# Optimization experiments

Hardware: AMD Instinct MI355X
Metric: run time of the kernel (lower is better)

The kernel has to match this reference:

```python
import jax, jax.numpy as jnp
import numpy as np

D_MODEL = 2048
N_HEADS = 32
N_KV = 8
HEAD_DIM = D_MODEL // N_HEADS  # 64
D_FF = 8192
ROPE_BASE = 10000.0
EPS = 1e-5
B, S = 2, 2048


def setup_inputs() -> dict:
    key = jax.random.key(0)
    ks = jax.random.split(key, 8)
    s = 0.02
    qkv_out = (N_HEADS + 2 * N_KV) * HEAD_DIM
    return {
        "x": jax.random.normal(ks[0], (B, S, D_MODEL), jnp.float32),
        "w_norm1": jnp.ones((D_MODEL,), jnp.float32),
        "w_qkv": jax.random.normal(ks[1], (D_MODEL, qkv_out), jnp.float32) * s,
        "w_out": jax.random.normal(ks[2], (D_MODEL, D_MODEL), jnp.float32) * s,
        "w_norm2": jnp.ones((D_MODEL,), jnp.float32),
        "w_gate": jax.random.normal(ks[3], (D_MODEL, D_FF), jnp.float32) * s,
        "w_up": jax.random.normal(ks[4], (D_MODEL, D_FF), jnp.float32) * s,
        "w_down": jax.random.normal(ks[5], (D_FF, D_MODEL), jnp.float32) * s,
    }


def _rmsnorm(x, w):
    var = jnp.mean(x * x, axis=-1, keepdims=True)
    return x * jax.lax.rsqrt(var + EPS) * w


def _rope(x, cos, sin):
    # x: [b, s, h, d]; cos/sin: [s, d/2]; non-interleaved (NeoX half split)
    half = x.shape[-1] // 2
    x1, x2 = x[..., :half], x[..., half:]
    c = cos[None, :, None, :]
    sn = sin[None, :, None, :]
    return jnp.concatenate([x1 * c - x2 * sn, x1 * sn + x2 * c], axis=-1)


def _forward(x, w_norm1, w_qkv, w_out, w_norm2, w_gate, w_up, w_down):
    b, s, d = x.shape
    # --- attention block ---
    h = _rmsnorm(x, w_norm1)
    qkv = h @ w_qkv  # [b, s, (H + 2*KV) * hd]
    q = qkv[..., : N_HEADS * HEAD_DIM].reshape(b, s, N_HEADS, HEAD_DIM)
    kv = qkv[..., N_HEADS * HEAD_DIM:].reshape(b, s, 2, N_KV, HEAD_DIM)
    k, v = kv[:, :, 0], kv[:, :, 1]

    inv_freq = 1.0 / (ROPE_BASE ** (jnp.arange(0, HEAD_DIM, 2, dtype=jnp.float32) / HEAD_DIM))
    t = jnp.arange(s, dtype=jnp.float32)
    freqs = t[:, None] * inv_freq[None, :]  # [s, hd/2]
    cos, sin = jnp.cos(freqs), jnp.sin(freqs)
    q = _rope(q, cos, sin)
    k = _rope(k, cos, sin)

    # GQA: repeat_interleave kv heads to match q heads
    g = N_HEADS // N_KV
    k = jnp.repeat(k, g, axis=2)  # [b, s, H, hd]
    v = jnp.repeat(v, g, axis=2)

    scale = 1.0 / np.sqrt(HEAD_DIM)
    scores = jnp.einsum("bqhd,bkhd->bhqk", q, k) * scale
    causal = jnp.tril(jnp.ones((s, s), bool))
    scores = jnp.where(causal[None, None], scores, jnp.finfo(scores.dtype).min)
    attn = jax.nn.softmax(scores, axis=-1)
    ctx = jnp.einsum("bhqk,bkhd->bqhd", attn, v).reshape(b, s, N_HEADS * HEAD_DIM)
    x = x + ctx @ w_out

    # --- MLP block (SwiGLU) ---
    h2 = _rmsnorm(x, w_norm2)
    mlp = (jax.nn.silu(h2 @ w_gate) * (h2 @ w_up)) @ w_down
    return x + mlp


def reference(x, w_norm1, w_qkv, w_out, w_norm2, w_gate, w_up, w_down):
    return _forward(x, w_norm1, w_qkv, w_out, w_norm2, w_gate, w_up, w_down)
```

## Files before the change

kernel.cpp:

```cpp
#include <hip/hip_runtime.h>
#include <stdint.h>

#define D_MODEL 2048
#define S_LEN   2048
#define NTOK    4096
#define QKV_N   3072
#define DFF     8192

typedef float  f32x4   __attribute__((ext_vector_type(4)));
typedef float  f32x16  __attribute__((ext_vector_type(16)));
typedef __bf16 bf16x8  __attribute__((ext_vector_type(8)));
typedef unsigned short u16;
typedef unsigned short u16x8 __attribute__((ext_vector_type(8)));

__device__ __forceinline__ float b2f(u16 u){ union{float f; uint32_t i;} v; v.i = ((uint32_t)u) << 16; return v.f; }
__device__ __forceinline__ u16 f2b(float f){
  union{float f; uint32_t i;} v; v.f = f;
  uint32_t r = v.i + 0x7FFFu + ((v.i >> 16) & 1u);
  return (u16)(r >> 16);
}

__device__ __forceinline__ void gload_lds16(const void* gsrc, void* ldst){
  __builtin_amdgcn_global_load_lds(
      (const __attribute__((address_space(1))) void*)gsrc,
      (__attribute__((address_space(3))) void*)ldst,
      16, 0, 0);
}

__device__ __forceinline__ void conv_tiles(const float* W, const float* W2, u16* WT,
    int Nfull, int Kt, int Nt, int k0g, int n0g, int rmul, void* ldsbuf)
{
  if (W == nullptr) return;
  float* tf = (float*)ldsbuf;
  const int tt  = threadIdx.x;
  const int nTn = Nt >> 6;
  const int nT  = (Kt >> 6) * nTn;
  const int bid = (blockIdx.z * gridDim.y + blockIdx.y) * gridDim.x + blockIdx.x;
  const int gsz = gridDim.x * gridDim.y * gridDim.z;
  const int c4 = (tt & 15) << 2;
  const int r  = tt >> 4;
  for (int tile = bid; tile < nT; tile += gsz) {
    const int k0 = (tile / nTn) << 6, n0 = (tile % nTn) << 6;
    for (int m = 0; m < 2; ++m) {
      const float* Ws = m ? W2 : W;
      if (m && W2 == nullptr) break;
      __syncthreads();
      if (tt < 256) {
#pragma unroll
        for (int i = 0; i < 4; ++i) {
          int row = r + i * 16;
          float4 v = *reinterpret_cast<const float4*>(&Ws[(size_t)(k0g + k0 + row) * Nfull + n0g + n0 + c4]);
          tf[row * 65 + c4 + 0] = v.x; tf[row * 65 + c4 + 1] = v.y;
          tf[row * 65 + c4 + 2] = v.z; tf[row * 65 + c4 + 3] = v.w;
        }
      }
      __syncthreads();
      if (tt < 256) {
#pragma unroll
        for (int i = 0; i < 4; ++i) {
          int n = r + i * 16;
          ushort4 ov;
          ov.x = f2b(tf[(c4 + 0) * 65 + n]); ov.y = f2b(tf[(c4 + 1) * 65 + n]);
          ov.z = f2b(tf[(c4 + 2) * 65 + n]); ov.w = f2b(tf[(c4 + 3) * 65 + n]);
          *reinterpret_cast<ushort4*>(&WT[(size_t)((n0 + n) * rmul + m) * Kt + k0 + c4]) = ov;
        }
      }
    }
  }
}

__global__ void sincos_kernel(float* __restrict__ ct, float* __restrict__ st)
{
  int idx = blockIdx.x * 256 + threadIdx.x;
  if (idx >= S_LEN * 32) return;
  int p = idx >> 5, i = idx & 31;
  double freq = pow(10000.0, -((double)(2*i)) / 64.0);
  double ang  = (double)p * freq;
  ct[idx] = (float)cos(ang);
  st[idx] = (float)sin(ang);
}

template<bool BF16IN>
__global__ __launch_bounds__(256) void rmsnorm_kernel(const void* __restrict__ xin, const float* __restrict__ w, u16* __restrict__ out,
                                                      const float* cvW, const float* cvW2, u16* cvWT, int cvNfull, int cvKt, int cvNt, int cvK0g, int cvN0g, int cvRm)
{
  __shared__ float tfbuf[64 * 65];
  const int row = blockIdx.x;
  const int t = threadIdx.x;
  float v[8];
  if (BF16IN) {
    const u16* xr = ((const u16*)xin) + (size_t)row * D_MODEL;
    u16x8 a = *reinterpret_cast<const u16x8*>(&xr[t*8]);
#pragma unroll
    for (int j = 0; j < 8; ++j) v[j] = b2f(a[j]);
  } else {
    const float* xr = ((const float*)xin) + (size_t)row * D_MODEL;
    float4 a = *reinterpret_cast<const float4*>(&xr[t*8]);
    float4 c = *reinterpret_cast<const float4*>(&xr[t*8+4]);
    v[0]=a.x; v[1]=a.y; v[2]=a.z; v[3]=a.w; v[4]=c.x; v[5]=c.y; v[6]=c.z; v[7]=c.w;
  }
  float ss = 0.f;
#pragma unroll
  for (int j = 0; j < 8; ++j) ss += v[j]*v[j];
#pragma unroll
  for (int d = 1; d < 64; d <<= 1) ss += __shfl_xor(ss, d);
  __shared__ float red[4];
  if ((t & 63) == 0) red[t >> 6] = ss;
  __syncthreads();
  ss = red[0] + red[1] + red[2] + red[3];
  const float sc = rsqrtf(ss * (1.0f / (float)D_MODEL) + 1e-5f);
  float4 w0 = *reinterpret_cast<const float4*>(&w[t*8]);
  float4 w1 = *reinterpret_cast<const float4*>(&w[t*8+4]);
  u16x8 o;
  o[0]=f2b(v[0]*sc*w0.x); o[1]=f2b(v[1]*sc*w0.y); o[2]=f2b(v[2]*sc*w0.z); o[3]=f2b(v[3]*sc*w0.w);
  o[4]=f2b(v[4]*sc*w1.x); o[5]=f2b(v[5]*sc*w1.y); o[6]=f2b(v[6]*sc*w1.z); o[7]=f2b(v[7]*sc*w1.w);
  *reinterpret_cast<u16x8*>(&out[(size_t)row * D_MODEL + t*8]) = o;
  conv_tiles(cvW, cvW2, cvWT, cvNfull, cvKt, cvNt, cvK0g, cvN0g, cvRm, tfbuf);
}

template<int EPI>
__device__ __forceinline__ void epi_store(size_t idx, float v, float* Cf, u16* Cb,
                                          const float* resf, const u16* resb, const u16* other)
{
  if (EPI == 2)      Cb[idx] = f2b(v / (1.0f + __expf(-v)));
  else if (EPI == 3) Cb[idx] = f2b(v * b2f(other[idx]));
  else if (EPI == 4) Cb[idx] = f2b(v);
  else if (EPI == 5) Cf[idx] += v;
  else if (EPI == 6) Cb[idx] = f2b(v + resf[idx]);
  else if (EPI == 7) Cf[idx] = v + b2f(resb[idx]);
  else if (EPI == 9) {
    float pv = __shfl_xor(v, 1);
    float gate = (threadIdx.x & 1) ? pv : v;
    float up   = (threadIdx.x & 1) ? v  : pv;
    if (!(threadIdx.x & 1)) Cb[idx] = f2b(gate / (1.0f + __expf(-gate)) * up);
  }
}

template<int EPI>
__global__ __launch_bounds__(512, 2) void gemm8p_kernel(
    const u16* __restrict__ A, const u16* __restrict__ BT, const u16* __restrict__ BT2,
    int K, int lda, int ldb, int ldc, int n_off,
    float* Cf, u16* Cb,
    const float* __restrict__ resf, const u16* __restrict__ resb, const u16* other,
    const float* cvW, const float* cvW2, u16* cvWT, int cvNfull, int cvKt, int cvNt, int cvK0g, int cvN0g, int cvRm)
{
  __shared__ u16 lds[65536];
  const int tid = threadIdx.x;
  const int w = tid >> 6, lane = tid & 63;
  const int g = lane >> 4, lr = lane & 15;
  const int wm = w >> 2, wn = w & 3;
  int fid = blockIdx.y * gridDim.x + blockIdx.x;
  const int nwg = gridDim.x * gridDim.y;
  fid = (fid & 7) * (nwg >> 3) + (fid >> 3);
  const int bn = fid / gridDim.y, bm = fid % gridDim.y;
  const int NT = K >> 6;
  const int NI = NT >> 1;

  const int srow = tid >> 3;
  const int sg   = (tid & 7) ^ (srow & 7);
  const u16* Asrc = A + (size_t)(bm * 256) * lda;
  const u16* Bsrc;
  if (EPI == 9) Bsrc = (bn < 16) ? BT + (size_t)(bn * 256) * ldb
                                 : BT2 + (size_t)(bn * 256 - 4096) * ldb;
  else          Bsrc = BT + (size_t)(bn * 256) * ldb;

  const int agc0 = ((0 + g) ^ (lr & 7)) * 8;
  const int agc1 = ((4 + g) ^ (lr & 7)) * 8;

  f32x4 acc[8][4];
#pragma unroll
  for (int i = 0; i < 8; ++i)
#pragma unroll
    for (int j = 0; j < 4; ++j) acc[i][j] = (f32x4){0.f, 0.f, 0.f, 0.f};
  bf16x8 af[4][2], bf0[2][2], bf1[2][2];

#define STAGE_H(isB, h, b, T) do {                                           \
    int tc = ((T) < NT) ? (T) : (NT - 1);                                    \
    const u16* sb = (isB) ? Bsrc : Asrc;                                     \
    const int  sld = (isB) ? ldb : lda;                                      \
    const u16* s0 = sb + (size_t)((h)*128 + srow) * sld + tc*64 + sg*8;      \
    u16* dst = &lds[(b)*32768 + (isB)*16384 + (h)*8192 + tid*8];             \
    gload_lds16(s0, dst);                                                    \
    gload_lds16(s0 + (size_t)64 * sld, dst + 4096);                          \
  } while (0)

#define LOADA(mih, b) { _Pragma("unroll") for (int q = 0; q < 4; ++q) {      \
    const u16* rp = &lds[(b)*32768 + (wm*128 + (mih)*64 + q*16 + lr) * 64];  \
    af[q][0] = *(const bf16x8*)(rp + agc0);                                  \
    af[q][1] = *(const bf16x8*)(rp + agc1); } }

#define LOADB(dst, nih, b) { _Pragma("unroll") for (int nq = 0; nq < 2; ++nq) { \
    const u16* rp = &lds[(b)*32768 + 16384 + (wn*64 + (nih)*32 + nq*16 + lr) * 64]; \
    dst[nq][0] = *(const bf16x8*)(rp + agc0);                                \
    dst[nq][1] = *(const bf16x8*)(rp + agc1); } }

#define MM(mih, nih, BF) {                                                   \
    __builtin_amdgcn_s_setprio(1);                                           \
    _Pragma("unroll") for (int kk = 0; kk < 2; ++kk)                         \
      _Pragma("unroll") for (int q = 0; q < 4; ++q)                          \
        _Pragma("unroll") for (int nq = 0; nq < 2; ++nq)                     \
          acc[(mih)*4+q][(nih)*2+nq] = __builtin_amdgcn_mfma_f32_16x16x32_bf16( \
              af[q][kk], BF[nq][kk], acc[(mih)*4+q][(nih)*2+nq], 0, 0, 0);   \
    __builtin_amdgcn_s_setprio(0); }

#define PHEND     __builtin_amdgcn_s_barrier();
#define PHEND_VM  asm volatile("s_waitcnt vmcnt(4)" ::: "memory");           \
                  __builtin_amdgcn_s_barrier();

  STAGE_H(0, 0, 0, 0); STAGE_H(0, 1, 0, 0);
  STAGE_H(1, 0, 0, 0); STAGE_H(1, 1, 0, 0);
  STAGE_H(1, 0, 1, 1); STAGE_H(1, 1, 1, 1);
  asm volatile("s_waitcnt vmcnt(4)" ::: "memory");
  __builtin_amdgcn_s_barrier();

  for (int i = 0; i < NI; ++i) {
    const int t0 = 2 * i;
    LOADA(0, 0); LOADB(bf0, 0, 0);
    STAGE_H(0, 0, 1, t0 + 1);
    MM(0, 0, bf0); PHEND;
    LOADB(bf1, 1, 0);
    STAGE_H(0, 1, 1, t0 + 1);
    MM(0, 1, bf1); PHEND;
    LOADA(1, 0);
    STAGE_H(1, 0, 0, t0 + 2);
    MM(1, 1, bf1); PHEND;
    STAGE_H(1, 1, 0, t0 + 2);
    MM(1, 0, bf0); PHEND_VM;
    LOADA(0, 1); LOADB(bf0, 0, 1);
    STAGE_H(0, 0, 0, t0 + 2);
    MM(0, 0, bf0); PHEND;
    LOADB(bf1, 1, 1);
    STAGE_H(0, 1, 0, t0 + 2);
    MM(0, 1, bf1); PHEND;
    LOADA(1, 1);
    STAGE_H(1, 0, 1, t0 + 3);
    MM(1, 1, bf1); PHEND;
    STAGE_H(1, 1, 1, t0 + 3);
    MM(1, 0, bf0); PHEND_VM;
  }
#undef STAGE_H
#undef LOADA
#undef LOADB
#undef MM

#pragma unroll
  for (int mi = 0; mi < 8; ++mi) {
    const int rowOff = (mi >> 2) * 64 + (mi & 3) * 16;
#pragma unroll
    for (int ni = 0; ni < 4; ++ni) {
      const int colOff = (ni >> 1) * 32 + (ni & 1) * 16;
#pragma unroll
      for (int j = 0; j < 4; ++j) {
        int row = bm*256 + wm*128 + rowOff + g*4 + j;
        int col = n_off + bn*256 + wn*64 + colOff + lr;
        size_t idx = (EPI == 9) ? ((size_t)row * ldc + (col >> 1))
                                : ((size_t)row * ldc + col);
        epi_store<EPI>(idx, acc[mi][ni][j], Cf, Cb, resf, resb, other);
      }
    }
  }
  conv_tiles(cvW, cvW2, cvWT, cvNfull, cvKt, cvNt, cvK0g, cvN0g, cvRm, lds);
}

template<int EPI>
__global__ __launch_bounds__(512) void gemm128_kernel(
    const u16* __restrict__ A, const u16* __restrict__ BT,
    int K, int lda, int ldb, int ldc, int n_off,
    float* Cf, u16* Cb,
    const float* __restrict__ resf, const u16* __restrict__ resb, const u16* other,
    const float* c1W, const float* c1W2, u16* c1WT, int c1Nfull, int c1Kt, int c1Nt, int c1K0g, int c1N0g, int c1Rm,
    const float* c2W, const float* c2W2, u16* c2WT, int c2Nfull, int c2Kt, int c2Nt, int c2K0g, int c2N0g, int c2Rm)
{
  __shared__ u16 lds[49152];
  const int tid = threadIdx.x;
  const int w = tid >> 6, lane = tid & 63;
  const int g = lane >> 4, lr = lane & 15;
  const int wm = w >> 2, wn = w & 3;
  int fid = blockIdx.y * gridDim.x + blockIdx.x;
  const int nwg = gridDim.x * gridDim.y;
  fid = (fid & 7) * (nwg >> 3) + (fid >> 3);
  const int bn = fid / gridDim.y, bm = fid % gridDim.y;
  const int NT = K >> 6;
  const int NI = NT >> 1;

  const int srow = tid >> 3;
  const int sg   = (tid & 7) ^ (srow & 7);
  const u16* Asrc = A  + (size_t)(bm * 128) * lda;
  const u16* Bsrc = BT + (size_t)(bn * 256) * ldb;

  const int agc0 = ((0 + g) ^ (lr & 7)) * 8;
  const int agc1 = ((4 + g) ^ (lr & 7)) * 8;

  f32x4 acc[4][4];
#pragma unroll
  for (int i = 0; i < 4; ++i)
#pragma unroll
    for (int j = 0; j < 4; ++j) acc[i][j] = (f32x4){0.f, 0.f, 0.f, 0.f};
  bf16x8 af[2][2], bf0[2][2], bf1[2][2];

#define STAGE_A(b, T) do {                                                   \
    int tc = ((T) < NT) ? (T) : (NT - 1);                                    \
    const u16* s0 = Asrc + (size_t)srow * lda + tc*64 + sg*8;                \
    u16* dst = &lds[(b)*24576 + tid*8];                                      \
    gload_lds16(s0, dst);                                                    \
    gload_lds16(s0 + (size_t)64 * lda, dst + 4096);                          \
  } while (0)

#define STAGE_BH(h, b, T) do {                                               \
    int tc = ((T) < NT) ? (T) : (NT - 1);                                    \
    const u16* s0 = Bsrc + (size_t)((h)*128 + srow) * ldb + tc*64 + sg*8;    \
    u16* dst = &lds[(b)*24576 + 8192 + (h)*8192 + tid*8];                    \
    gload_lds16(s0, dst);                                                    \
    gload_lds16(s0 + (size_t)64 * ldb, dst + 4096);                         \
  } while (0)

#define LOADA(mih, b) { _Pragma("unroll") for (int q = 0; q < 2; ++q) {      \
    const u16* rp = &lds[(b)*24576 + (wm*64 + (mih)*32 + q*16 + lr) * 64];   \
    af[q][0] = *(const bf16x8*)(rp + agc0);                                  \
    af[q][1] = *(const bf16x8*)(rp + agc1); } }

#define LOADB(dst, nih, b) { _Pragma("unroll") for (int nq = 0; nq < 2; ++nq) { \
    const u16* rp = &lds[(b)*24576 + 8192 + (wn*64 + (nih)*32 + nq*16 + lr) * 64]; \
    dst[nq][0] = *(const bf16x8*)(rp + agc0);                                \
    dst[nq][1] = *(const bf16x8*)(rp + agc1); } }

#define MM(mih, nih, BF) {                                                   \
    __builtin_amdgcn_s_setprio(1);                                           \
    _Pragma("unroll") for (int kk = 0; kk < 2; ++kk)                         \
      _Pragma("unroll") for (int q = 0; q < 2; ++q)                          \
        _Pragma("unroll") for (int nq = 0; nq < 2; ++nq)                     \
          acc[(mih)*2+q][(nih)*2+nq] = __builtin_amdgcn_mfma_f32_16x16x32_bf16( \
              af[q][kk], BF[nq][kk], acc[(mih)*2+q][(nih)*2+nq], 0, 0, 0);   \
    __builtin_amdgcn_s_setprio(0); }

#define PHEND     __builtin_amdgcn_s_barrier();

  STAGE_A(0, 0); STAGE_BH(0, 0, 0); STAGE_BH(1, 0, 0);
  STAGE_BH(0, 1, 1); STAGE_BH(1, 1, 1);
  asm volatile("s_waitcnt vmcnt(4)" ::: "memory");
  __builtin_amdgcn_s_barrier();

  for (int i = 0; i < NI; ++i) {
    const int t0 = 2 * i;
    LOADA(0, 0); LOADB(bf0, 0, 0);
    STAGE_A(1, t0 + 1);
    MM(0, 0, bf0); PHEND;
    LOADB(bf1, 1, 0);
    STAGE_BH(0, 0, t0 + 2);
    MM(0, 1, bf1); PHEND;
    LOADA(1, 0);
    STAGE_BH(1, 0, t0 + 2);
    MM(1, 1, bf1); PHEND;
    STAGE_A(0, t0 + 2);
    MM(1, 0, bf0);
    asm volatile("s_waitcnt vmcnt(6)" ::: "memory");
    __builtin_amdgcn_s_barrier();
    LOADA(0, 1); LOADB(bf0, 0, 1);
    MM(0, 0, bf0); PHEND;
    LOADB(bf1, 1, 1);
    STAGE_BH(0, 1, t0 + 3);
    MM(0, 1, bf1); PHEND;
    LOADA(1, 1);
    STAGE_BH(1, 1, t0 + 3);
    MM(1, 1, bf1); PHEND;
    MM(1, 0, bf0);
    asm volatile("s_waitcnt vmcnt(4)" ::: "memory");
    __builtin_amdgcn_s_barrier();
  }
#undef STAGE_A
#undef STAGE_BH
#undef LOADA
#undef LOADB
#undef MM
#undef PHEND

#pragma unroll
  for (int mi = 0; mi < 4; ++mi) {
    const int rowOff = (mi >> 1) * 32 + (mi & 1) * 16;
#pragma unroll
    for (int ni = 0; ni < 4; ++ni) {
      const int colOff = (ni >> 1) * 32 + (ni & 1) * 16;
#pragma unroll
      for (int j = 0; j < 4; ++j) {
        int row = bm*128 + wm*64 + rowOff + g*4 + j;
        int col = n_off + bn*256 + wn*64 + colOff + lr;
        epi_store<EPI>((size_t)row * ldc + col, acc[mi][ni][j], Cf, Cb, resf, resb, other);
      }
    }
  }
  conv_tiles(c1W, c1W2, c1WT, c1Nfull, c1Kt, c1Nt, c1K0g, c1N0g, c1Rm, lds);
  conv_tiles(c2W, c2W2, c2WT, c2Nfull, c2Kt, c2Nt, c2K0g, c2N0g, c2Rm, lds);
}

__global__ __launch_bounds__(256) void rope_kernel(
    const u16* __restrict__ qkv, const float* __restrict__ ct, const float* __restrict__ st,
    u16* __restrict__ Kt, u16* __restrict__ VT)
{
  const int tok = blockIdx.x;
  const int b = tok >> 11, s = tok & (S_LEN - 1);
  const int w = threadIdx.x >> 6, lane = threadIdx.x & 63;
  const size_t base = (size_t)tok * QKV_N;
  for (int slot = w; slot < 16; slot += 4) {
    int col = (slot < 8) ? 2048 + slot * 64 : 2560 + (slot - 8) * 64;
    float v = b2f(qkv[base + col + lane]);
    if (slot < 8) {
      int i = lane & 31;
      float c = ct[s * 32 + i], sn = st[s * 32 + i];
      float p = b2f(qkv[base + col + (lane ^ 32)]);
      v = (lane < 32) ? (v * c - p * sn) : (v * c + p * sn);
    }
    u16 ob = f2b(v);
    if (slot < 8) Kt[((size_t)(b * 8 + slot)     * S_LEN + s) * 64 + lane] = ob;
    else          VT[((size_t)(b * 8 + slot - 8) * 64 + lane) * S_LEN + s] = ob;
  }
}

#define ASCALE 0.1803368801111204f
#define MFIX   16.0f
__global__ __launch_bounds__(256, 2) void attn_kernel(
    const u16* __restrict__ qkv, const u16* __restrict__ Kt,
    const u16* __restrict__ VT, u16* __restrict__ ctx,
    const float* __restrict__ ct, const float* __restrict__ st,
    const float* cvW, const float* cvW2, u16* cvWT, int cvNfull, int cvKt, int cvNt, int cvK0g, int cvN0g, int cvRm)
{
  __shared__ float tfbuf[64 * 65];
  const int fid = blockIdx.y * gridDim.x + blockIdx.x;
  const int idx = fid >> 3;
  const int bh  = (fid & 7) * 8 + (idx & 7);
  const int y   = idx >> 3;
  const int wid = threadIdx.x >> 6;
  const int lane = threadIdx.x & 63;
  const int b = bh >> 5, h = bh & 31;
  const int kvh = (b << 3) + (h >> 2);
  const int jj = y * 4 + wid;
  const int cq = lane & 31;
  const int hi = lane >> 5;

  const u16* Kp = Kt + (size_t)kvh * S_LEN * 64 + cq * 64 + hi * 8;
  const u16* Vbase = VT + (size_t)kvh * 64 * S_LEN + hi * 8;
  const u16* Vp[4];
#pragma unroll
  for (int v = 0; v < 4; ++v)
    Vp[v] = Vbase + (size_t)((v & 1) * 32 + cq) * S_LEN + (v >> 1) * 16;

  __shared__ float xch[4][32];

#define ATT_LOADK(KF, T) { _Pragma("unroll") for (int q_ = 0; q_ < 4; ++q_) \
    KF[q_] = *(const bf16x8*)(Kp + (T) * 2048 + q_ * 16); }
#define ATT_LOADV(VF, T) { _Pragma("unroll") for (int v_ = 0; v_ < 4; ++v_) \
    VF[v_] = *(const bf16x8*)(Vp[v_] + (T) * 32); }

#define ATT_QK(S, KF) do {                                                   \
    S = (f32x16){};                                                          \
    S = __builtin_amdgcn_mfma_f32_32x32x16_bf16(KF[0], qf[0], S, 0, 0, 0);   \
    S = __builtin_amdgcn_mfma_f32_32x32x16_bf16(KF[1], qf[1], S, 0, 0, 0);   \
    S = __builtin_amdgcn_mfma_f32_32x32x16_bf16(KF[2], qf[2], S, 0, 0, 0);   \
    S = __builtin_amdgcn_mfma_f32_32x32x16_bf16(KF[3], qf[3], S, 0, 0, 0);   \
  } while (0)

#define ATT_PACK(P, PA0, PA1) do {                                           \
    uint32_t wds[8], pw[8];                                                  \
    _Pragma("unroll") for (int j = 0; j < 8; ++j) {                          \
      uint32_t wv;                                                           \
      asm("v_cvt_pk_bf16_f32 %0, %1, %2" : "=v"(wv) : "v"((P)[2*j]), "v"((P)[2*j+1])); \
      wds[j] = wv;                                                           \
    }                                                                        \
    _Pragma("unroll") for (int j = 0; j < 8; ++j) pw[j] = __shfl_xor(wds[j], 32); \
    PA0.u[0] = hi ? pw[2]  : wds[0];                                         \
    PA0.u[1] = hi ? pw[3]  : wds[1];                                         \
    PA0.u[2] = hi ? wds[2] : pw[0];                                          \
    PA0.u[3] = hi ? wds[3] : pw[1];                                          \
    PA1.u[0] = hi ? pw[6]  : wds[4];                                         \
    PA1.u[1] = hi ? pw[7]  : wds[5];                                         \
    PA1.u[2] = hi ? wds[6] : pw[4];                                          \
    PA1.u[3] = hi ? wds[7] : pw[5];                                          \
  } while (0)

#define ATT_FIN1(S, VF) do {                                                 \
    float p[16];                                                             \
    _Pragma("unroll") for (int r = 0; r < 16; ++r) p[r] = S[r];              \
    _Pragma("unroll") for (int r = 0; r < 16; ++r) {                         \
      int kk = (r & 3) + 8 * (r >> 2) + 4 * hi;                              \
      if (kk > cq) p[r] = -1e30f;                                            \
    }                                                                        \
    float ts_ = 0.f;                                                         \
    _Pragma("unroll") for (int r = 0; r < 16; ++r) { p[r] = exp2f(p[r] - MFIX); ts_ += p[r]; } \
    l += ts_;                                                                \
    union { uint32_t u[4]; bf16x8 v; } pa0, pa1;                             \
    ATT_PACK(p, pa0, pa1);                                                   \
    o0 = __builtin_amdgcn_mfma_f32_32x32x16_bf16(pa0.v, VF[0], o0, 0, 0, 0); \
    o0 = __builtin_amdgcn_mfma_f32_32x32x16_bf16(pa1.v, VF[2], o0, 0, 0, 0); \
    o1 = __builtin_amdgcn_mfma_f32_32x32x16_bf16(pa0.v, VF[1], o1, 0, 0, 0); \
    o1 = __builtin_amdgcn_mfma_f32_32x32x16_bf16(pa1.v, VF[3], o1, 0, 0, 0); \
  } while (0)

#define ATT_FIN2(SA, SB, VFA, VFB, MASKB) do {                               \
    float p[32];                                                             \
    _Pragma("unroll") for (int r = 0; r < 16; ++r) { p[r] = SA[r]; p[16+r] = SB[r]; } \
    if (MASKB) {                                                             \
      _Pragma("unroll") for (int r = 0; r < 16; ++r) {                       \
        int kk = (r & 3) + 8 * (r >> 2) + 4 * hi;                            \
        if (kk > cq) p[16+r] = -1e30f;                                       \
      }                                                                      \
    }                                                                        \
    _Pragma("unroll") for (int r = 0; r < 32; ++r) p[r] = exp2f(p[r] - MFIX); \
    {                                                                        \
      float s1_ = 0.f, s2_ = 0.f;                                            \
      _Pragma("unroll") for (int r = 0; r < 16; ++r) { s1_ += p[r]; s2_ += p[16+r]; } \
      l += s1_ + s2_;                                                        \
    }                                                                        \
    union { uint32_t u[4]; bf16x8 v; } pa0, pa1, pb0, pb1;                   \
    ATT_PACK(p, pa0, pa1);                                                   \
    ATT_PACK((p + 16), pb0, pb1);                                            \
    o0 = __builtin_amdgcn_mfma_f32_32x32x16_bf16(pa0.v, VFA[0], o0, 0, 0, 0); \
    o0 = __builtin_amdgcn_mfma_f32_32x32x16_bf16(pa1.v, VFA[2], o0, 0, 0, 0); \
    o1 = __builtin_amdgcn_mfma_f32_32x32x16_bf16(pa0.v, VFA[1], o1, 0, 0, 0); \
    o1 = __builtin_amdgcn_mfma_f32_32x32x16_bf16(pa1.v, VFA[3], o1, 0, 0, 0); \
    o0 = __builtin_amdgcn_mfma_f32_32x32x16_bf16(pb0.v, VFB[0], o0, 0, 0, 0); \
    o0 = __builtin_amdgcn_mfma_f32_32x32x16_bf16(pb1.v, VFB[2], o0, 0, 0, 0); \
    o1 = __builtin_amdgcn_mfma_f32_32x32x16_bf16(pb0.v, VFB[1], o1, 0, 0, 0); \
    o1 = __builtin_amdgcn_mfma_f32_32x32x16_bf16(pb1.v, VFB[3], o1, 0, 0, 0); \
  } while (0)

#pragma unroll 1
  for (int task = 0; task < 2; ++task) {
    const int qt = task ? (63 - jj) : jj;
    const int q0 = qt << 5;
    const int nt = qt + 1;

    bf16x8 qf[4];
    {
      const u16* Qr = qkv + (size_t)(b * S_LEN + q0 + cq) * QKV_N + h * 64 + hi * 8;
      u16 qr[4][8];
#pragma unroll
      for (int t = 0; t < 4; ++t)
        *reinterpret_cast<u16x8*>(qr[t]) = *reinterpret_cast<const u16x8*>(Qr + t * 16);
      const float* cb = ct + (size_t)(q0 + cq) * 32 + hi * 8;
      const float* sb = st + (size_t)(q0 + cq) * 32 + hi * 8;
      union { u16 u[8]; bf16x8 v; } qo[4];
#pragma unroll
      for (int t = 0; t < 2; ++t) {
        float4 c0 = *reinterpret_cast<const float4*>(cb + 16 * t);
        float4 c1 = *reinterpret_cast<const float4*>(cb + 16 * t + 4);
        float4 s0 = *reinterpret_cast<const float4*>(sb + 16 * t);
        float4 s1 = *reinterpret_cast<const float4*>(sb + 16 * t + 4);
        float cc[8] = {c0.x,c0.y,c0.z,c0.w, c1.x,c1.y,c1.z,c1.w};
        float ssn[8] = {s0.x,s0.y,s0.z,s0.w, s1.x,s1.y,s1.z,s1.w};
#pragma unroll
        for (int i = 0; i < 8; ++i) {
          float lo = b2f(qr[t][i]), hif = b2f(qr[t + 2][i]);
          qo[t].u[i]     = f2b((lo * cc[i] - hif * ssn[i]) * ASCALE);
          qo[t + 2].u[i] = f2b((hif * cc[i] + lo * ssn[i]) * ASCALE);
        }
      }
#pragma unroll
      for (int t = 0; t < 4; ++t) qf[t] = qo[t].v;
    }

    f32x16 o0 = {}, o1 = {};
    float l = 0.f;

    const int npair = nt >> 1;
    bf16x8 kfA[4], kfB[4], vfA[4], vfB[4];

#pragma unroll 1
    for (int i = 0; i < npair; ++i) {
      const int Ta = 2 * i, Tb = 2 * i + 1;
      ATT_LOADK(kfA, Ta); ATT_LOADK(kfB, Tb);
      ATT_LOADV(vfA, Ta); ATT_LOADV(vfB, Tb);
      f32x16 sA, sB;
      ATT_QK(sA, kfA); ATT_QK(sB, kfB);
      ATT_FIN2(sA, sB, vfA, vfB, (Tb == nt - 1));
    }
    if (nt & 1) {
      const int T = nt - 1;
      ATT_LOADK(kfA, T); ATT_LOADV(vfA, T);
      f32x16 sA;
      ATT_QK(sA, kfA);
      ATT_FIN1(sA, vfA);
    }

    l += __shfl_xor(l, 32);
    float linv = 1.0f / l;
    if (hi == 0) xch[wid][cq] = linv;
    asm volatile("s_waitcnt lgkmcnt(0)" ::: "memory");
    __builtin_amdgcn_sched_barrier(0);
    float4 n0 = *reinterpret_cast<const float4*>(&xch[wid][4 * hi + 0]);
    float4 n1 = *reinterpret_cast<const float4*>(&xch[wid][4 * hi + 8]);
    float4 n2 = *reinterpret_cast<const float4*>(&xch[wid][4 * hi + 16]);
    float4 n3 = *reinterpret_cast<const float4*>(&xch[wid][4 * hi + 24]);
    float na[16] = {n0.x,n0.y,n0.z,n0.w, n1.x,n1.y,n1.z,n1.w,
                    n2.x,n2.y,n2.z,n2.w, n3.x,n3.y,n3.z,n3.w};
#pragma unroll
    for (int r = 0; r < 16; ++r) {
      int row = (r & 3) + 8 * (r >> 2) + 4 * hi;
      size_t base = (size_t)(b * S_LEN + q0 + row) * D_MODEL + h * 64;
      ctx[base + cq]      = f2b(o0[r] * na[r]);
      ctx[base + 32 + cq] = f2b(o1[r] * na[r]);
    }
  }
#undef ATT_LOADK
#undef ATT_LOADV
#undef ATT_QK
#undef ATT_PACK
#undef ATT_FIN1
#undef ATT_FIN2

  conv_tiles(cvW, cvW2, cvWT, cvNfull, cvKt, cvNt, cvK0g, cvN0g, cvRm, tfbuf);
}

#define NOCV nullptr, nullptr, nullptr, 0, 0, 0, 0, 0, 1
extern "C" void kernel_launch(void* const* d_in, const int* in_sizes, int n_in,
                              void* d_out, int out_size, void* d_ws, size_t ws_size,
                              hipStream_t stream)
{
  const float* x     = (const float*)d_in[0];
  const float* wn1   = (const float*)d_in[1];
  const float* wqkv  = (const float*)d_in[2];
  const float* wout  = (const float*)d_in[3];
  const float* wn2   = (const float*)d_in[4];
  const float* wgate = (const float*)d_in[5];
  const float* wup   = (const float*)d_in[6];
  const float* wdown = (const float*)d_in[7];
  float* out = (float*)d_out;
  char* ws = (char*)d_ws;

  float* cosT = (float*)(ws + 0);
  float* sinT = (float*)(ws + 262144);
  u16*   U1   = (u16*)  (ws + 524288);
  u16*   U2   = (u16*)  (ws + 17301504);
  u16*   x1b  = (u16*)  (ws + 34078720);
  char*  S    = ws + 50855936;
  u16*   hB   = (u16*)(S + 0);
  u16*   qkvB = (u16*)(S + 16777216);
  u16*   kB   = (u16*)(S + 41943040);
  u16*   vtB  = (u16*)(S + 46137344);
  u16*   ctxB = (u16*)(S + 0);
  u16*   h2B  = (u16*)(S + 0);
  u16*   slab = (u16*)(S + 16777216);
  u16*   U7   = (u16*)(S + 50331648);

  sincos_kernel<<<dim3(256), 256, 0, stream>>>(cosT, sinT);
  rmsnorm_kernel<false><<<dim3(NTOK), 256, 0, stream>>>(x, wn1, hB,
      wqkv, nullptr, U1, 3072, 2048, 3072, 0, 0, 1);

  gemm128_kernel<4><<<dim3(12, 32), 512, 0, stream>>>(hB, U1, 2048, 2048, 2048, 3072, 0,
      nullptr, qkvB, nullptr, nullptr, nullptr,
      wout, nullptr, U7, 2048, 2048, 2048, 0, 0, 1, NOCV);
  rope_kernel<<<dim3(NTOK), 256, 0, stream>>>(qkvB, cosT, sinT, kB, vtB);
  attn_kernel<<<dim3(64, 8), 256, 0, stream>>>(qkvB, kB, vtB, ctxB, cosT, sinT,
      wgate, wup, U1, 8192, 2048, 2048, 0, 0, 2);

  gemm128_kernel<6><<<dim3(8, 32), 512, 0, stream>>>(ctxB, U7, 2048, 2048, 2048, 2048, 0,
      nullptr, x1b, x, nullptr, nullptr,
      wgate, wup, U2, 8192, 2048, 2048, 0, 2048, 2, NOCV);

  rmsnorm_kernel<true><<<dim3(NTOK), 256, 0, stream>>>(x1b, wn2, h2B,
      wdown, nullptr, U7, 2048, 4096, 2048, 0, 0, 1);

  gemm8p_kernel<9><<<dim3(32, 16), 512, 0, stream>>>(h2B, U1, U2, 2048, 2048, 2048, 4096, 0,
      nullptr, slab, nullptr, nullptr, nullptr, NOCV);
  gemm128_kernel<7><<<dim3(8, 32), 512, 0, stream>>>(slab, U7, 4096, 4096, 4096, 2048, 0,
      out, nullptr, nullptr, x1b, nullptr,
      wgate, wup, U1, 8192, 2048, 2048, 0, 4096, 2,
      wgate, wup, U2, 8192, 2048, 2048, 0, 6144, 2);
  gemm8p_kernel<9><<<dim3(32, 16), 512, 0, stream>>>(h2B, U1, U2, 2048, 2048, 2048, 4096, 0,
      nullptr, slab, nullptr, nullptr, nullptr,
      wdown, nullptr, U7, 2048, 4096, 2048, 4096, 0, 1);
  gemm128_kernel<5><<<dim3(8, 32), 512, 0, stream>>>(slab, U7, 4096, 4096, 4096, 2048, 0,
      out, nullptr, nullptr, nullptr, nullptr, NOCV, NOCV);
}
```

Measured before the change: 766.8 us.

## Fuse paired causal query tiles to share K/V loads in attention

Each wave previously handled its two balanced query tiles (jj and 63-jj) one after the other, loading K and V separately for each. Now both tiles' Q fragments are loaded up front and a single loop over key tiles runs, so every K/V fragment is loaded once and used by both query tiles. This removes redundant global K/V traffic but drops the two-tile unroll that gave more instruction-level parallelism. It also doubles the live accumulator registers, which may lower occupancy.

```diff
diff --git a/kernel.cpp b/kernel.cpp
--- a/kernel.cpp
+++ b/kernel.cpp
@@ -436,6 +436,9 @@
   const int cq = lane & 31;
   const int hi = lane >> 5;
 
+  const int q0a = jj << 5,        nta = jj + 1;
+  const int q0b = (63 - jj) << 5, ntb = 64 - jj;
+
   const u16* Kp = Kt + (size_t)kvh * S_LEN * 64 + cq * 64 + hi * 8;
   const u16* Vbase = VT + (size_t)kvh * 64 * S_LEN + hi * 8;
   const u16* Vp[4];
@@ -450,12 +453,12 @@
 #define ATT_LOADV(VF, T) { _Pragma("unroll") for (int v_ = 0; v_ < 4; ++v_) \
     VF[v_] = *(const bf16x8*)(Vp[v_] + (T) * 32); }
 
-#define ATT_QK(S, KF) do {                                                   \
+#define ATT_QK(S, KF, QF) do {                                               \
     S = (f32x16){};                                                          \
-    S = __builtin_amdgcn_mfma_f32_32x32x16_bf16(KF[0], qf[0], S, 0, 0, 0);   \
-    S = __builtin_amdgcn_mfma_f32_32x32x16_bf16(KF[1], qf[1], S, 0, 0, 0);   \
-    S = __builtin_amdgcn_mfma_f32_32x32x16_bf16(KF[2], qf[2], S, 0, 0, 0);   \
-    S = __builtin_amdgcn_mfma_f32_32x32x16_bf16(KF[3], qf[3], S, 0, 0, 0);   \
+    S = __builtin_amdgcn_mfma_f32_32x32x16_bf16(KF[0], QF[0], S, 0, 0, 0);   \
+    S = __builtin_amdgcn_mfma_f32_32x32x16_bf16(KF[1], QF[1], S, 0, 0, 0);   \
+    S = __builtin_amdgcn_mfma_f32_32x32x16_bf16(KF[2], QF[2], S, 0, 0, 0);   \
+    S = __builtin_amdgcn_mfma_f32_32x32x16_bf16(KF[3], QF[3], S, 0, 0, 0);   \
   } while (0)
 
 #define ATT_PACK(P, PA0, PA1) do {                                           \
@@ -476,135 +479,100 @@
     PA1.u[3] = hi ? wds[7] : pw[5];                                          \
   } while (0)
 
-#define ATT_FIN1(S, VF) do {                                                 \
+#define ATT_FIN(S, VF, O0, O1, L, MASK) do {                                 \
     float p[16];                                                             \
     _Pragma("unroll") for (int r = 0; r < 16; ++r) p[r] = S[r];              \
-    _Pragma("unroll") for (int r = 0; r < 16; ++r) {                         \
-      int kk = (r & 3) + 8 * (r >> 2) + 4 * hi;                              \
-      if (kk > cq) p[r] = -1e30f;                                            \
+    if (MASK) {                                                              \
+      _Pragma("unroll") for (int r = 0; r < 16; ++r) {                       \
+        int kk = (r & 3) + 8 * (r >> 2) + 4 * hi;                            \
+        if (kk > cq) p[r] = -1e30f;                                          \
+      }                                                                      \
     }                                                                        \
     float ts_ = 0.f;                                                         \
     _Pragma("unroll") for (int r = 0; r < 16; ++r) { p[r] = exp2f(p[r] - MFIX); ts_ += p[r]; } \
-    l += ts_;                                                                \
+    L += ts_;                                                                \
     union { uint32_t u[4]; bf16x8 v; } pa0, pa1;                             \
     ATT_PACK(p, pa0, pa1);                                                   \
-    o0 = __builtin_amdgcn_mfma_f32_32x32x16_bf16(pa0.v, VF[0], o0, 0, 0, 0); \
-    o0 = __builtin_amdgcn_mfma_f32_32x32x16_bf16(pa1.v, VF[2], o0, 0, 0, 0); \
-    o1 = __builtin_amdgcn_mfma_f32_32x32x16_bf16(pa0.v, VF[1], o1, 0, 0, 0); \
-    o1 = __builtin_amdgcn_mfma_f32_32x32x16_bf16(pa1.v, VF[3], o1, 0, 0, 0); \
-  } while (0)
-
-#define ATT_FIN2(SA, SB, VFA, VFB, MASKB) do {                               \
-    float p[32];                                                             \
-    _Pragma("unroll") for (int r = 0; r < 16; ++r) { p[r] = SA[r]; p[16+r] = SB[r]; } \
-    if (MASKB) {                                                             \
-      _Pragma("unroll") for (int r = 0; r < 16; ++r) {                       \
-        int kk = (r & 3) + 8 * (r >> 2) + 4 * hi;                            \
-        if (kk > cq) p[16+r] = -1e30f;                                       \
+    O0 = __builtin_amdgcn_mfma_f32_32x32x16_bf16(pa0.v, VF[0], O0, 0, 0, 0); \
+    O0 = __builtin_amdgcn_mfma_f32_32x32x16_bf16(pa1.v, VF[2], O0, 0, 0, 0); \
+    O1 = __builtin_amdgcn_mfma_f32_32x32x16_bf16(pa0.v, VF[1], O1, 0, 0, 0); \
+    O1 = __builtin_amdgcn_mfma_f32_32x32x16_bf16(pa1.v, VF[3], O1, 0, 0, 0); \
+  } while (0)
+
+#define ATT_LOADQ(QF, Q0) do {                                               \
+    const u16* Qr = qkv + (size_t)(b * S_LEN + (Q0) + cq) * QKV_N + h * 64 + hi * 8; \
+    u16 qr[4][8];                                                            \
+    _Pragma("unroll") for (int t = 0; t < 4; ++t)                            \
+      *reinterpret_cast<u16x8*>(qr[t]) = *reinterpret_cast<const u16x8*>(Qr + t * 16); \
+    const float* cb = ct + (size_t)((Q0) + cq) * 32 + hi * 8;                \
+    const float* sb = st + (size_t)((Q0) + cq) * 32 + hi * 8;                \
+    union { u16 u[8]; bf16x8 v; } qo[4];                                     \
+    _Pragma("unroll") for (int t = 0; t < 2; ++t) {                          \
+      float4 c0 = *reinterpret_cast<const float4*>(cb + 16 * t);             \
+      float4 c1 = *reinterpret_cast<const float4*>(cb + 16 * t + 4);         \
+      float4 s0 = *reinterpret_cast<const float4*>(sb + 16 * t);             \
+      float4 s1 = *reinterpret_cast<const float4*>(sb + 16 * t + 4);         \
+      float cc[8] = {c0.x,c0.y,c0.z,c0.w, c1.x,c1.y,c1.z,c1.w};              \
+      float ssn[8] = {s0.x,s0.y,s0.z,s0.w, s1.x,s1.y,s1.z,s1.w};             \
+      _Pragma("unroll") for (int i = 0; i < 8; ++i) {                        \
+        float lo = b2f(qr[t][i]), hif = b2f(qr[t + 2][i]);                   \
+        qo[t].u[i]     = f2b((lo * cc[i] - hif * ssn[i]) * ASCALE);          \
+        qo[t + 2].u[i] = f2b((hif * cc[i] + lo * ssn[i]) * ASCALE);          \
       }                                                                      \
     }                                                                        \
-    _Pragma("unroll") for (int r = 0; r < 32; ++r) p[r] = exp2f(p[r] - MFIX); \
-    {                                                                        \
-      float s1_ = 0.f, s2_ = 0.f;                                            \
-      _Pragma("unroll") for (int r = 0; r < 16; ++r) { s1_ += p[r]; s2_ += p[16+r]; } \
-      l += s1_ + s2_;                                                        \
+    _Pragma("unroll") for (int t = 0; t < 4; ++t) QF[t] = qo[t].v;           \
+  } while (0)
+
+#define ATT_EPI(O0, O1, L, Q0) do {                                          \
+    float lv = (L) + __shfl_xor((L), 32);                                    \
+    float linv = 1.0f / lv;                                                  \
+    if (hi == 0) xch[wid][cq] = linv;                                        \
+    asm volatile("s_waitcnt lgkmcnt(0)" ::: "memory");                       \
+    __builtin_amdgcn_sched_barrier(0);                                       \
+    float4 n0 = *reinterpret_cast<const float4*>(&xch[wid][4 * hi + 0]);     \
+    float4 n1 = *reinterpret_cast<const float4*>(&xch[wid][4 * hi + 8]);     \
+    float4 n2 = *reinterpret_cast<const float4*>(&xch[wid][4 * hi + 16]);    \
+    float4 n3 = *reinterpret_cast<const float4*>(&xch[wid][4 * hi + 24]);    \
+    float na[16] = {n0.x,n0.y,n0.z,n0.w, n1.x,n1.y,n1.z,n1.w,                \
+                    n2.x,n2.y,n2.z,n2.w, n3.x,n3.y,n3.z,n3.w};               \
+    _Pragma("unroll") for (int r = 0; r < 16; ++r) {                         \
+      int row = (r & 3) + 8 * (r >> 2) + 4 * hi;                             \
+      size_t base_ = (size_t)(b * S_LEN + (Q0) + row) * D_MODEL + h * 64;    \
+      ctx[base_ + cq]      = f2b(O0[r] * na[r]);                             \
+      ctx[base_ + 32 + cq] = f2b(O1[r] * na[r]);                             \
     }                                                                        \
-    union { uint32_t u[4]; bf16x8 v; } pa0, pa1, pb0, pb1;                   \
-    ATT_PACK(p, pa0, pa1);                                                   \
-    ATT_PACK((p + 16), pb0, pb1);                                            \
-    o0 = __builtin_amdgcn_mfma_f32_32x32x16_bf16(pa0.v, VFA[0], o0, 0, 0, 0); \
-    o0 = __builtin_amdgcn_mfma_f32_32x32x16_bf16(pa1.v, VFA[2], o0, 0, 0, 0); \
-    o1 = __builtin_amdgcn_mfma_f32_32x32x16_bf16(pa0.v, VFA[1], o1, 0, 0, 0); \
-    o1 = __builtin_amdgcn_mfma_f32_32x32x16_bf16(pa1.v, VFA[3], o1, 0, 0, 0); \
-    o0 = __builtin_amdgcn_mfma_f32_32x32x16_bf16(pb0.v, VFB[0], o0, 0, 0, 0); \
-    o0 = __builtin_amdgcn_mfma_f32_32x32x16_bf16(pb1.v, VFB[2], o0, 0, 0, 0); \
-    o1 = __builtin_amdgcn_mfma_f32_32x32x16_bf16(pb0.v, VFB[1], o1, 0, 0, 0); \
-    o1 = __builtin_amdgcn_mfma_f32_32x32x16_bf16(pb1.v, VFB[3], o1, 0, 0, 0); \
-  } while (0)
-
+  } while (0)
+
+  bf16x8 qfA[4], qfB[4];
+  ATT_LOADQ(qfA, q0a);
+  ATT_LOADQ(qfB, q0b);
+
+  f32x16 oA0 = {}, oA1 = {}, oB0 = {}, oB1 = {};
+  float lA = 0.f, lB = 0.f;
+
+  bf16x8 kf[4], vf[4];
 #pragma unroll 1
-  for (int task = 0; task < 2; ++task) {
-    const int qt = task ? (63 - jj) : jj;
-    const int q0 = qt << 5;
-    const int nt = qt + 1;
-
-    bf16x8 qf[4];
-    {
-      const u16* Qr = qkv + (size_t)(b * S_LEN + q0 + cq) * QKV_N + h * 64 + hi * 8;
-      u16 qr[4][8];
-#pragma unroll
-      for (int t = 0; t < 4; ++t)
-        *reinterpret_cast<u16x8*>(qr[t]) = *reinterpret_cast<const u16x8*>(Qr + t * 16);
-      const float* cb = ct + (size_t)(q0 + cq) * 32 + hi * 8;
-      const float* sb = st + (size_t)(q0 + cq) * 32 + hi * 8;
-      union { u16 u[8]; bf16x8 v; } qo[4];
-#pragma unroll
-      for (int t = 0; t < 2; ++t) {
-        float4 c0 = *reinterpret_cast<const float4*>(cb + 16 * t);
-        float4 c1 = *reinterpret_cast<const float4*>(cb + 16 * t + 4);
-        float4 s0 = *reinterpret_cast<const float4*>(sb + 16 * t);
-        float4 s1 = *reinterpret_cast<const float4*>(sb + 16 * t + 4);
-        float cc[8] = {c0.x,c0.y,c0.z,c0.w, c1.x,c1.y,c1.z,c1.w};
-        float ssn[8] = {s0.x,s0.y,s0.z,s0.w, s1.x,s1.y,s1.z,s1.w};
-#pragma unroll
-        for (int i = 0; i < 8; ++i) {
-          float lo = b2f(qr[t][i]), hif = b2f(qr[t + 2][i]);
-          qo[t].u[i]     = f2b((lo * cc[i] - hif * ssn[i]) * ASCALE);
-          qo[t + 2].u[i] = f2b((hif * cc[i] + lo * ssn[i]) * ASCALE);
-        }
-      }
-#pragma unroll
-      for (int t = 0; t < 4; ++t) qf[t] = qo[t].v;
-    }
-
-    f32x16 o0 = {}, o1 = {};
-    float l = 0.f;
-
-    const int npair = nt >> 1;
-    bf16x8 kfA[4], kfB[4], vfA[4], vfB[4];
-
-#pragma unroll 1
-    for (int i = 0; i < npair; ++i) {
-      const int Ta = 2 * i, Tb = 2 * i + 1;
-      ATT_LOADK(kfA, Ta); ATT_LOADK(kfB, Tb);
-      ATT_LOADV(vfA, Ta); ATT_LOADV(vfB, Tb);
-      f32x16 sA, sB;
-      ATT_QK(sA, kfA); ATT_QK(sB, kfB);
-      ATT_FIN2(sA, sB, vfA, vfB, (Tb == nt - 1));
-    }
-    if (nt & 1) {
-      const int T = nt - 1;
-      ATT_LOADK(kfA, T); ATT_LOADV(vfA, T);
-      f32x16 sA;
-      ATT_QK(sA, kfA);
-      ATT_FIN1(sA, vfA);
-    }
-
-    l += __shfl_xor(l, 32);
-    float linv = 1.0f / l;
-    if (hi == 0) xch[wid][cq] = linv;
-    asm volatile("s_waitcnt lgkmcnt(0)" ::: "memory");
-    __builtin_amdgcn_sched_barrier(0);
-    float4 n0 = *reinterpret_cast<const float4*>(&xch[wid][4 * hi + 0]);
-    float4 n1 = *reinterpret_cast<const float4*>(&xch[wid][4 * hi + 8]);
-    float4 n2 = *reinterpret_cast<const float4*>(&xch[wid][4 * hi + 16]);
-    float4 n3 = *reinterpret_cast<const float4*>(&xch[wid][4 * hi + 24]);
-    float na[16] = {n0.x,n0.y,n0.z,n0.w, n1.x,n1.y,n1.z,n1.w,
-                    n2.x,n2.y,n2.z,n2.w, n3.x,n3.y,n3.z,n3.w};
-#pragma unroll
-    for (int r = 0; r < 16; ++r) {
-      int row = (r & 3) + 8 * (r >> 2) + 4 * hi;
-      size_t base = (size_t)(b * S_LEN + q0 + row) * D_MODEL + h * 64;
-      ctx[base + cq]      = f2b(o0[r] * na[r]);
-      ctx[base + 32 + cq] = f2b(o1[r] * na[r]);
-    }
-  }
+  for (int t = 0; t < ntb; ++t) {
+    ATT_LOADK(kf, t);
+    ATT_LOADV(vf, t);
+    const bool doA = (t < nta);
+    f32x16 sA, sB;
+    if (doA) ATT_QK(sA, kf, qfA);
+    ATT_QK(sB, kf, qfB);
+    if (doA) ATT_FIN(sA, vf, oA0, oA1, lA, (t == nta - 1));
+    ATT_FIN(sB, vf, oB0, oB1, lB, (t == ntb - 1));
+  }
+
+  ATT_EPI(oA0, oA1, lA, q0a);
+  ATT_EPI(oB0, oB1, lB, q0b);
+
 #undef ATT_LOADK
 #undef ATT_LOADV
 #undef ATT_QK
 #undef ATT_PACK
-#undef ATT_FIN1
-#undef ATT_FIN2
+#undef ATT_FIN
+#undef ATT_LOADQ
+#undef ATT_EPI
 
   conv_tiles(cvW, cvW2, cvWT, cvNfull, cvKt, cvNt, cvK0g, cvN0g, cvRm, tfbuf);
 }
```

New measurement: 748.6 us. -2.4%, faster.
